# Kernel tuning notes

Hardware: AMD Instinct MI355X
Metric: run time of the kernel (lower is better)

Reference implementation:

```python
import jax, jax.numpy as jnp
import numpy as np
from jax import lax

BN_EPS = 1e-5

def _maxpool_same(x, k):
    # x: [B, C, H, W]; stride-1 max pool with 'same' padding (pad value -inf, like torch)
    p = k // 2
    neg_inf = jnp.array(-jnp.inf, dtype=x.dtype)
    return lax.reduce_window(x, neg_inf, lax.max,
                             window_dimensions=(1, 1, k, k),
                             window_strides=(1, 1, 1, 1),
                             padding=[(0, 0), (0, 0), (p, p), (p, p)])

def setup_inputs() -> dict:
    key = jax.random.key(0)
    k1, k2 = jax.random.split(key)
    B, Cin, Cout, H, W_ = 16, 1024, 512, 32, 32
    x = jax.random.normal(k1, (B, Cin, H, W_), dtype=jnp.float32)
    W = jax.random.normal(k2, (Cout, Cin), dtype=jnp.float32) * (1.0 / np.sqrt(Cin))
    gamma = jnp.ones((Cout,), dtype=jnp.float32)
    beta = jnp.zeros((Cout,), dtype=jnp.float32)
    running_mean = jnp.zeros((Cout,), dtype=jnp.float32)
    running_var = jnp.ones((Cout,), dtype=jnp.float32)
    return {"x": x, "W": W, "gamma": gamma, "beta": beta,
            "running_mean": running_mean, "running_var": running_var}

def reference(x, W, gamma, beta, running_mean, running_var):
    # 1x1 conv (no bias): [B, Cin, H, W] x [Cout, Cin] -> [B, Cout, H, W]
    y = jnp.einsum('bchw,oc->bohw', x, W)
    # BatchNorm (inference form with running stats)
    inv = gamma * lax.rsqrt(running_var + BN_EPS)
    y = y * inv[None, :, None, None] + (beta - running_mean * inv)[None, :, None, None]
    # Mish activation
    y = y * jnp.tanh(jax.nn.softplus(y))
    # Three overlapping stride-1 max pools, concat channel-wise: [m13, m9, m5, y]
    return jnp.concatenate([_maxpool_same(y, 13), _maxpool_same(y, 9),
                            _maxpool_same(y, 5), y], axis=1)
```

## Files before the change

### kernel.cpp

```cpp
#include <hip/hip_runtime.h>
#include <hip/hip_bf16.h>
#include <math.h>

typedef __attribute__((ext_vector_type(4))) float  f32x4;
typedef __attribute__((ext_vector_type(8))) __bf16 bf16x8;
typedef __attribute__((ext_vector_type(4))) __bf16 bf16x4;
typedef __attribute__((ext_vector_type(2))) __bf16 bf16x2;

#define BN_EPS 1e-5f

__device__ __forceinline__ void gload16(const void* g, void* l) {
    __builtin_amdgcn_global_load_lds(
        (const __attribute__((address_space(1))) unsigned int*)g,
        (__attribute__((address_space(3))) unsigned int*)l, 16, 0, 0);
}

__global__ __launch_bounds__(256) void prep_kernel(
    const float* __restrict__ W, const float* __restrict__ gamma,
    const float* __restrict__ beta, const float* __restrict__ rmean,
    const float* __restrict__ rvar, __bf16* __restrict__ Wb,
    float* __restrict__ sc, float* __restrict__ bs)
{
    int t = blockIdx.x * 256 + threadIdx.x;
    int idx = t * 4;
    f32x4 v = *(const f32x4*)(W + idx);
    bf16x4 o;
    o[0] = (__bf16)v[0]; o[1] = (__bf16)v[1];
    o[2] = (__bf16)v[2]; o[3] = (__bf16)v[3];
    *(bf16x4*)(Wb + idx) = o;
    if (t < 512) {
        float s = gamma[t] * rsqrtf(rvar[t] + BN_EPS);
        sc[t] = s;
        bs[t] = beta[t] - rmean[t] * s;
    }
}

__global__ __launch_bounds__(256) void transpose_kernel(
    const float* __restrict__ x, __bf16* __restrict__ xt)
{
    __shared__ float lt[64][65];
    const int t = threadIdx.x;
    const int b = blockIdx.y;
    const int c0  = (blockIdx.x & 15) * 64;
    const int hw0 = (blockIdx.x >> 4) * 64;

    const int cl = t >> 4;
    const int q  = (t & 15) * 4;
    const float* src = x + (((size_t)(b * 1024 + c0 + cl)) << 10) + hw0 + q;
    #pragma unroll
    for (int i = 0; i < 4; ++i) {
        f32x4 v = *(const f32x4*)(src + ((size_t)i << 14));
        int c = cl + i * 16;
        lt[c][q + 0] = v[0]; lt[c][q + 1] = v[1];
        lt[c][q + 2] = v[2]; lt[c][q + 3] = v[3];
    }
    __syncthreads();
    const int cc = (t & 31) * 2;
    const int h0 = t >> 5;
    #pragma unroll
    for (int i = 0; i < 8; ++i) {
        int hw = h0 + i * 8;
        bf16x2 p;
        p[0] = (__bf16)lt[cc][hw];
        p[1] = (__bf16)lt[cc + 1][hw];
        *(bf16x2*)(xt + (((size_t)(b * 1024 + hw0 + hw)) << 10) + c0 + cc) = p;
    }
}

__global__ __launch_bounds__(256, 2) void gemm_kernel(
    const __bf16* __restrict__ Wb,
    const __bf16* __restrict__ xt,
    const float* __restrict__ sc, const float* __restrict__ bs,
    float* __restrict__ out)
{
    __shared__ __align__(16) char lds[32768];
    char* const Alds = lds;
    char* const Blds = lds + 16384;

    const int t  = threadIdx.x;
    const int o0  = blockIdx.x * 128;
    const int hw0 = blockIdx.y * 128;
    const int b   = blockIdx.z;

    const int srow = t >> 3;
    const int sswz = ((t & 7) ^ ((t >> 3) & 7)) * 16;
    const char* Ag = (const char*)Wb + (((size_t)(o0 + srow)) << 11) + sswz;
    const char* Bg = (const char*)xt + ((size_t)b << 21)
                   + (((size_t)(hw0 + srow)) << 11) + sswz;
    char* Al = Alds + t * 16;
    char* Bl = Blds + t * 16;

    const int l  = t & 63;
    const int lr = l & 15;
    const int lk = l >> 4;
    const int wm = (t >> 6) & 1;
    const int wn = t >> 7;

    int aoff[4][2], boff[4][2];
    #pragma unroll
    for (int i = 0; i < 4; ++i)
        #pragma unroll
        for (int kk = 0; kk < 2; ++kk) {
            int ra = wm * 64 + i * 16 + lr;
            int rb = wn * 64 + i * 16 + lr;
            int s  = lk + kk * 4;
            aoff[i][kk] = ra * 128 + ((s ^ (ra & 7)) * 16);
            boff[i][kk] = rb * 128 + ((s ^ (rb & 7)) * 16);
        }

    f32x4 acc[4][4] = {};

    for (int ks = 0; ks < 16; ++ks) {
        __syncthreads();
        const int kb = ks * 128;
        #pragma unroll
        for (int i = 0; i < 4; ++i) {
            gload16(Ag + (i << 16) + kb, Al + (i << 12));
            gload16(Bg + (i << 16) + kb, Bl + (i << 12));
        }
        __syncthreads();
        bf16x8 af[4][2], bfr[4][2];
        #pragma unroll
        for (int i = 0; i < 4; ++i)
            #pragma unroll
            for (int kk = 0; kk < 2; ++kk) {
                af[i][kk]  = *(const bf16x8*)(Alds + aoff[i][kk]);
                bfr[i][kk] = *(const bf16x8*)(Blds + boff[i][kk]);
            }
        #pragma unroll
        for (int kk = 0; kk < 2; ++kk)
            #pragma unroll
            for (int i = 0; i < 4; ++i)
                #pragma unroll
                for (int j = 0; j < 4; ++j)
                    acc[i][j] = __builtin_amdgcn_mfma_f32_16x16x32_bf16(
                        af[i][kk], bfr[j][kk], acc[i][j], 0, 0, 0);
    }

    const size_t outbase = (((size_t)b * 2048 + 1536) << 10);
    #pragma unroll
    for (int i = 0; i < 4; ++i) {
        const int ob = o0 + wm * 64 + i * 16 + lk * 4;
        const f32x4 s4 = *(const f32x4*)(sc + ob);
        const f32x4 b4 = *(const f32x4*)(bs + ob);
        #pragma unroll
        for (int r = 0; r < 4; ++r) {
            float* orow = out + outbase + (((size_t)(ob + r)) << 10)
                        + hw0 + wn * 64 + lr;
            #pragma unroll
            for (int j = 0; j < 4; ++j) {
                float v = acc[i][j][r] * s4[r] + b4[r];
                float e   = __expf(fminf(v, 15.0f));
                float num = e * (e + 2.0f);
                orow[j * 16] = v * (num / (num + 2.0f));
            }
        }
    }
}

__global__ __launch_bounds__(256) void pool_kernel(float* __restrict__ out)
{
    __shared__ float A[32][33];
    __shared__ float B[32][33];
    const int t = threadIdx.x;
    const int b = blockIdx.x >> 9;
    const int o = blockIdx.x & 511;
    const int r  = t >> 3;
    const int c0 = (t & 7) * 4;

    const size_t ybase = ((size_t)(b * 2048 + 1536 + o)) << 10;
    f32x4 v = *(const f32x4*)(out + ybase + t * 4);
    A[r][c0] = v[0]; A[r][c0 + 1] = v[1]; A[r][c0 + 2] = v[2]; A[r][c0 + 3] = v[3];
    __syncthreads();

    for (int p = 0; p < 3; ++p) {
        float wv[8];
        #pragma unroll
        for (int k = 0; k < 8; ++k) {
            int c = c0 - 2 + k;
            wv[k] = (c >= 0 && c < 32) ? A[r][c] : -INFINITY;
        }
        #pragma unroll
        for (int q = 0; q < 4; ++q) {
            float h = fmaxf(fmaxf(fmaxf(wv[q], wv[q + 1]), fmaxf(wv[q + 2], wv[q + 3])), wv[q + 4]);
            B[r][c0 + q] = h;
        }
        __syncthreads();
        f32x4 m;
        m[0] = m[1] = m[2] = m[3] = -INFINITY;
        #pragma unroll
        for (int k = 0; k < 5; ++k) {
            int rr = r - 2 + k;
            if (rr >= 0 && rr < 32) {
                m[0] = fmaxf(m[0], B[rr][c0]);
                m[1] = fmaxf(m[1], B[rr][c0 + 1]);
                m[2] = fmaxf(m[2], B[rr][c0 + 2]);
                m[3] = fmaxf(m[3], B[rr][c0 + 3]);
            }
        }
        A[r][c0] = m[0]; A[r][c0 + 1] = m[1]; A[r][c0 + 2] = m[2]; A[r][c0 + 3] = m[3];
        const size_t obase = ((size_t)(b * 2048 + (2 - p) * 512 + o)) << 10;
        *(f32x4*)(out + obase + t * 4) = m;
        __syncthreads();
    }
}

extern "C" void kernel_launch(void* const* d_in, const int* in_sizes, int n_in,
                              void* d_out, int out_size, void* d_ws, size_t ws_size,
                              hipStream_t stream)
{
    const float* x     = (const float*)d_in[0];
    const float* W     = (const float*)d_in[1];
    const float* gamma = (const float*)d_in[2];
    const float* beta  = (const float*)d_in[3];
    const float* rmean = (const float*)d_in[4];
    const float* rvar  = (const float*)d_in[5];
    float* out = (float*)d_out;
    char*  ws  = (char*)d_ws;

    __bf16* xt = (__bf16*)ws;
    __bf16* Wb = (__bf16*)(ws + 33554432);
    float*  sc = (float*)(ws + 34603008);
    float*  bs = (float*)(ws + 34605056);

    prep_kernel<<<512, 256, 0, stream>>>(W, gamma, beta, rmean, rvar, Wb, sc, bs);
    transpose_kernel<<<dim3(256, 16), 256, 0, stream>>>(x, xt);
    gemm_kernel<<<dim3(4, 8, 16), 256, 0, stream>>>(Wb, xt, sc, bs, out);
    pool_kernel<<<8192, 256, 0, stream>>>(out);
}
```

Before: 77.26 us.

## Fuse input transpose/bf16 conversion into GEMM using LDS transpose reads

Removes the separate transpose kernel that wrote a bf16 [B,HW,C] copy of x. The GEMM now loads fp32 x tiles straight from global memory, converts them to bf16 into a custom LDS layout, and builds the B fragments with ds_read_b64_tr_b16 transposing LDS reads. This drops a 64MB read plus 32MB write pass and one launch. In exchange the GEMM reads fp32 x directly from global (twice the bytes of bf16, and re-read by each of the 4 output-channel blocks), with synchronous register loads instead of async LDS loads, which may expose latency.

```diff
diff --git a/kernel.cpp b/kernel.cpp
--- a/kernel.cpp
+++ b/kernel.cpp
@@ -5,7 +5,6 @@
 typedef __attribute__((ext_vector_type(4))) float  f32x4;
 typedef __attribute__((ext_vector_type(8))) __bf16 bf16x8;
 typedef __attribute__((ext_vector_type(4))) __bf16 bf16x4;
-typedef __attribute__((ext_vector_type(2))) __bf16 bf16x2;
 
 #define BN_EPS 1e-5f
 
@@ -13,6 +12,14 @@
     __builtin_amdgcn_global_load_lds(
         (const __attribute__((address_space(1))) unsigned int*)g,
         (__attribute__((address_space(3))) unsigned int*)l, 16, 0, 0);
+}
+
+__device__ __forceinline__ bf16x4 tr_read(const char* p) {
+    bf16x4 d;
+    asm volatile("ds_read_b64_tr_b16 %0, %1"
+                 : "=v"(d)
+                 : "v"((const __attribute__((address_space(3))) char*)p));
+    return d;
 }
 
 __global__ __launch_bounds__(256) void prep_kernel(
@@ -35,47 +42,15 @@
     }
 }
 
-__global__ __launch_bounds__(256) void transpose_kernel(
-    const float* __restrict__ x, __bf16* __restrict__ xt)
-{
-    __shared__ float lt[64][65];
-    const int t = threadIdx.x;
-    const int b = blockIdx.y;
-    const int c0  = (blockIdx.x & 15) * 64;
-    const int hw0 = (blockIdx.x >> 4) * 64;
-
-    const int cl = t >> 4;
-    const int q  = (t & 15) * 4;
-    const float* src = x + (((size_t)(b * 1024 + c0 + cl)) << 10) + hw0 + q;
-    #pragma unroll
-    for (int i = 0; i < 4; ++i) {
-        f32x4 v = *(const f32x4*)(src + ((size_t)i << 14));
-        int c = cl + i * 16;
-        lt[c][q + 0] = v[0]; lt[c][q + 1] = v[1];
-        lt[c][q + 2] = v[2]; lt[c][q + 3] = v[3];
-    }
-    __syncthreads();
-    const int cc = (t & 31) * 2;
-    const int h0 = t >> 5;
-    #pragma unroll
-    for (int i = 0; i < 8; ++i) {
-        int hw = h0 + i * 8;
-        bf16x2 p;
-        p[0] = (__bf16)lt[cc][hw];
-        p[1] = (__bf16)lt[cc + 1][hw];
-        *(bf16x2*)(xt + (((size_t)(b * 1024 + hw0 + hw)) << 10) + c0 + cc) = p;
-    }
-}
-
 __global__ __launch_bounds__(256, 2) void gemm_kernel(
     const __bf16* __restrict__ Wb,
-    const __bf16* __restrict__ xt,
+    const float* __restrict__ x,
     const float* __restrict__ sc, const float* __restrict__ bs,
     float* __restrict__ out)
 {
     __shared__ __align__(16) char lds[32768];
     char* const Alds = lds;
-    char* const Blds = lds + 16384;
+    char* const Bld  = lds + 16384;
 
     const int t  = threadIdx.x;
     const int o0  = blockIdx.x * 128;
@@ -85,27 +60,35 @@
     const int srow = t >> 3;
     const int sswz = ((t & 7) ^ ((t >> 3) & 7)) * 16;
     const char* Ag = (const char*)Wb + (((size_t)(o0 + srow)) << 11) + sswz;
-    const char* Bg = (const char*)xt + ((size_t)b << 21)
-                   + (((size_t)(hw0 + srow)) << 11) + sswz;
     char* Al = Alds + t * 16;
-    char* Bl = Blds + t * 16;
+
+    int bto[8];
+    int gxo[8];
+    #pragma unroll
+    for (int it = 0; it < 8; ++it) {
+        int idx = t + (it << 8);
+        int hwq = idx & 31, c = idx >> 5, cq = c >> 2;
+        int pos = ((((hwq >> 2) << 1) + (cq >> 3)) * 2 + (cq & 1)) * 4 + ((cq >> 1) & 3);
+        bto[it] = (pos << 7) + ((c & 3) << 5) + ((hwq & 3) << 3);
+        gxo[it] = (c << 10) + (hwq << 2);
+    }
+    const float* xs = x + (((size_t)b) << 20) + hw0;
 
     const int l  = t & 63;
     const int lr = l & 15;
     const int lk = l >> 4;
     const int wm = (t >> 6) & 1;
     const int wn = t >> 7;
-
-    int aoff[4][2], boff[4][2];
+    const char* Btr = Bld + wn * 8192 + l * 8;
+
+    int aoff[4][2];
     #pragma unroll
     for (int i = 0; i < 4; ++i)
         #pragma unroll
         for (int kk = 0; kk < 2; ++kk) {
             int ra = wm * 64 + i * 16 + lr;
-            int rb = wn * 64 + i * 16 + lr;
             int s  = lk + kk * 4;
             aoff[i][kk] = ra * 128 + ((s ^ (ra & 7)) * 16);
-            boff[i][kk] = rb * 128 + ((s ^ (rb & 7)) * 16);
         }
 
     f32x4 acc[4][4] = {};
@@ -114,19 +97,44 @@
         __syncthreads();
         const int kb = ks * 128;
         #pragma unroll
-        for (int i = 0; i < 4; ++i) {
+        for (int i = 0; i < 4; ++i)
             gload16(Ag + (i << 16) + kb, Al + (i << 12));
-            gload16(Bg + (i << 16) + kb, Bl + (i << 12));
-        }
-        __syncthreads();
+
+        const float* xk = xs + ((size_t)(ks * 64) << 10);
+        f32x4 xv[8];
+        #pragma unroll
+        for (int it = 0; it < 8; ++it)
+            xv[it] = *(const f32x4*)(xk + gxo[it]);
+        #pragma unroll
+        for (int it = 0; it < 8; ++it) {
+            bf16x4 w;
+            w[0] = (__bf16)xv[it][0]; w[1] = (__bf16)xv[it][1];
+            w[2] = (__bf16)xv[it][2]; w[3] = (__bf16)xv[it][3];
+            *(bf16x4*)(Bld + bto[it]) = w;
+        }
+        __syncthreads();
+
         bf16x8 af[4][2], bfr[4][2];
         #pragma unroll
         for (int i = 0; i < 4; ++i)
             #pragma unroll
+            for (int kk = 0; kk < 2; ++kk)
+                af[i][kk] = *(const bf16x8*)(Alds + aoff[i][kk]);
+        #pragma unroll
+        for (int j = 0; j < 4; ++j)
+            #pragma unroll
             for (int kk = 0; kk < 2; ++kk) {
-                af[i][kk]  = *(const bf16x8*)(Alds + aoff[i][kk]);
-                bfr[i][kk] = *(const bf16x8*)(Blds + boff[i][kk]);
+                const char* p = Btr + ((j * 2 + kk) << 10);
+                bf16x4 t0 = tr_read(p);
+                bf16x4 t1 = tr_read(p + 512);
+                bf16x8 f;
+                f[0] = t0[0]; f[1] = t0[1]; f[2] = t0[2]; f[3] = t0[3];
+                f[4] = t1[0]; f[5] = t1[1]; f[6] = t1[2]; f[7] = t1[3];
+                bfr[j][kk] = f;
             }
+        asm volatile("s_waitcnt lgkmcnt(0)" ::: "memory");
+        __builtin_amdgcn_sched_barrier(0);
+
         #pragma unroll
         for (int kk = 0; kk < 2; ++kk)
             #pragma unroll
@@ -218,13 +226,11 @@
     float* out = (float*)d_out;
     char*  ws  = (char*)d_ws;
 
-    __bf16* xt = (__bf16*)ws;
-    __bf16* Wb = (__bf16*)(ws + 33554432);
-    float*  sc = (float*)(ws + 34603008);
-    float*  bs = (float*)(ws + 34605056);
+    __bf16* Wb = (__bf16*)ws;
+    float*  sc = (float*)(ws + 1048576);
+    float*  bs = (float*)(ws + 1050624);
 
     prep_kernel<<<512, 256, 0, stream>>>(W, gamma, beta, rmean, rvar, Wb, sc, bs);
-    transpose_kernel<<<dim3(256, 16), 256, 0, stream>>>(x, xt);
-    gemm_kernel<<<dim3(4, 8, 16), 256, 0, stream>>>(Wb, xt, sc, bs, out);
+    gemm_kernel<<<dim3(4, 8, 16), 256, 0, stream>>>(Wb, x, sc, bs, out);
     pool_kernel<<<8192, 256, 0, stream>>>(out);
 }
```

After: 84.14 us. 1.09x slower.
